# Performance work log

Hardware: AMD Instinct MI355X
Metric: run time of the kernel (lower is better)

The kernel has to match this reference:

```python
import jax, jax.numpy as jnp
import numpy as np
from jax import lax

NUM_STATES = 1024
NUM_OBS = 512
BATCH = 64
SEQ = 128


def setup_inputs() -> dict:
    key = jax.random.key(0)
    k1, k2, k3, k4 = jax.random.split(key, 4)
    value = jax.random.randint(k1, (BATCH, SEQ), 0, NUM_OBS)  # int observation ids
    prior_logits = jax.random.normal(k2, (NUM_STATES,), dtype=jnp.float32)
    trans_logits = jax.random.normal(k3, (NUM_STATES, NUM_STATES), dtype=jnp.float32)
    emission_logits = jax.random.normal(k4, (NUM_STATES, NUM_OBS), dtype=jnp.float32)
    return {"value": value, "prior_logits": prior_logits,
            "trans_logits": trans_logits, "emission_logits": emission_logits}


def reference(value, prior_logits, trans_logits, emission_logits):
    # Categorical(...).logits in torch is log-normalized: logits - logsumexp(logits)
    prior_ln = jax.nn.log_softmax(prior_logits)                 # [S]
    trans_ln = jax.nn.log_softmax(trans_logits, axis=-1)        # [S_from, S_to], row-normalized
    emis_ln = jax.nn.log_softmax(emission_logits, axis=-1)      # [S, V]
    transT = trans_ln.T                                         # [S_to, S_from]

    # Per-timestep emission log-likelihoods: emis_ln[:, value] -> [S, B, T] -> [T, B, S]
    e = jnp.transpose(emis_ln[:, value], (2, 1, 0))

    alpha0 = e[0] + prior_ln                                    # [B, S]

    def step(alpha, e_t):
        # alpha_new[b, j] = e_t[b, j] + logsumexp_i(transT[j, i] + alpha[b, i])
        a = e_t + jax.nn.logsumexp(transT[None, :, :] + alpha[:, None, :], axis=2)
        return a, None

    alpha_final, _ = lax.scan(step, alpha0, e[1:])
    return jax.nn.logsumexp(alpha_final, axis=1)                # [B]
```

## Files before the change

### kernel.cpp

```cpp
#include <hip/hip_runtime.h>
#include <hip/hip_bf16.h>


typedef __attribute__((ext_vector_type(8))) short short8;
typedef __attribute__((ext_vector_type(4))) float f32x4;

__device__ __forceinline__ float bf2f(short x) {
  unsigned u = ((unsigned)(unsigned short)x) << 16;
  return __builtin_bit_cast(float, u);
}
__device__ __forceinline__ short f2bf(float f) {
  unsigned u = __builtin_bit_cast(unsigned, f);
  u += 0x7fffu + ((u >> 16) & 1u);
  return (short)(u >> 16);
}
__device__ __forceinline__ float waveReduceMax(float v) {
  #pragma unroll
  for (int d = 1; d < 64; d <<= 1) v = fmaxf(v, __shfl_xor(v, d, 64));
  return v;
}
__device__ __forceinline__ float waveReduceSum(float v) {
  #pragma unroll
  for (int d = 1; d < 64; d <<= 1) v += __shfl_xor(v, d, 64);
  return v;
}

__device__ __forceinline__ void store_bf16_coh(short* p, short v) {
  asm volatile("global_store_short %0, %1, off sc0 sc1" :: "v"(p), "v"(v) : "memory");
}
__device__ __forceinline__ void store_u32_coh(unsigned* p, unsigned v) {
  asm volatile("global_store_dword %0, %1, off sc0 sc1" :: "v"(p), "v"(v) : "memory");
}
__device__ __forceinline__ unsigned load_u32_coh(const unsigned* p) {
  unsigned r;
  asm volatile("global_load_dword %0, %1, off sc0 sc1\n\ts_waitcnt vmcnt(0)"
               : "=v"(r) : "v"(p) : "memory");
  return r;
}
__device__ __forceinline__ short8 load_short8_coh(const short* p) {
  short8 r;
  asm volatile("global_load_dwordx4 %0, %1, off sc0 sc1\n\ts_waitcnt vmcnt(0)"
               : "=v"(r) : "v"(p) : "memory");
  return r;
}


__global__ __launch_bounds__(256) void k_rowstat(const float* __restrict__ x,
                                                 float* __restrict__ rstat) {
  __shared__ float sm[8];
  const int row = blockIdx.x;
  const float* p = x + row * 1024;
  const int tid = threadIdx.x;
  float m = -1e30f;
  for (int i = tid; i < 1024; i += 256) m = fmaxf(m, p[i]);
  m = waveReduceMax(m);
  if ((tid & 63) == 0) sm[tid >> 6] = m;
  __syncthreads();
  m = fmaxf(fmaxf(sm[0], sm[1]), fmaxf(sm[2], sm[3]));
  float s = 0.f;
  for (int i = tid; i < 1024; i += 256) s += __expf(p[i] - m);
  s = waveReduceSum(s);
  if ((tid & 63) == 0) sm[4 + (tid >> 6)] = s;
  __syncthreads();
  if (tid == 0) {
    float tot = sm[4] + sm[5] + sm[6] + sm[7];
    rstat[row * 2] = m;
    rstat[row * 2 + 1] = 1.0f / tot;
  }
}

__global__ __launch_bounds__(256) void k_fillP(const float* __restrict__ trans,
                                               const float* __restrict__ rstat,
                                               short* __restrict__ P_frag) {
  __shared__ float st[512];
  const int w = blockIdx.x, tid = threadIdx.x;
  for (int kk = 0; kk < 32; ++kk) {
    for (int idx = tid; idx < 512; idx += 256) {
      int il = idx >> 4, jl = idx & 15;
      int i = kk * 32 + il, j = w * 16 + jl;
      float m = rstat[i * 2], invs = rstat[i * 2 + 1];
      st[idx] = __expf(trans[i * 1024 + j] - m) * invs;
    }
    __syncthreads();
    for (int idx = tid; idx < 512; idx += 256) {
      int lane = idx >> 3, e = idx & 7;
      int il = ((lane >> 4) & 3) * 8 + e, jl = lane & 15;
      P_frag[w * 16384 + kk * 512 + idx] = f2bf(st[il * 16 + jl]);
    }
    __syncthreads();
  }
}

__global__ __launch_bounds__(256) void k_emis(const float* __restrict__ x,
                                              short* __restrict__ o) {
  __shared__ float sm[8];
  const int row = blockIdx.x;
  const float* p = x + row * 512;
  const int tid = threadIdx.x;
  float m = -1e30f;
  for (int i = tid; i < 512; i += 256) m = fmaxf(m, p[i]);
  m = waveReduceMax(m);
  if ((tid & 63) == 0) sm[tid >> 6] = m;
  __syncthreads();
  m = fmaxf(fmaxf(sm[0], sm[1]), fmaxf(sm[2], sm[3]));
  float s = 0.f;
  for (int i = tid; i < 512; i += 256) s += __expf(p[i] - m);
  s = waveReduceSum(s);
  if ((tid & 63) == 0) sm[4 + (tid >> 6)] = s;
  __syncthreads();
  float invs = 512.0f / (sm[4] + sm[5] + sm[6] + sm[7]);
  for (int i = tid; i < 512; i += 256)
    o[i * 1024 + row] = f2bf(__expf(p[i] - m) * invs);
}

__global__ __launch_bounds__(256) void k_prior(const float* __restrict__ x,
                                               float* __restrict__ o) {
  __shared__ float sm[8];
  const int tid = threadIdx.x;
  float m = -1e30f;
  for (int i = tid; i < 1024; i += 256) m = fmaxf(m, x[i]);
  m = waveReduceMax(m);
  if ((tid & 63) == 0) sm[tid >> 6] = m;
  __syncthreads();
  m = fmaxf(fmaxf(sm[0], sm[1]), fmaxf(sm[2], sm[3]));
  float s = 0.f;
  for (int i = tid; i < 1024; i += 256) s += __expf(x[i] - m);
  s = waveReduceSum(s);
  if ((tid & 63) == 0) sm[4 + (tid >> 6)] = s;
  __syncthreads();
  float invs = 1.0f / (sm[4] + sm[5] + sm[6] + sm[7]);
  for (int i = tid; i < 1024; i += 256) o[i] = __expf(x[i] - m) * invs;
}


#define LA(OFF) asm volatile("global_load_dwordx4 %0, %1, off offset:" #OFF " sc0 sc1" \
                             : "=v"(a[OFF / 64]) : "v"(ab) : "memory")

__global__ __launch_bounds__(256, 1) void hmm_main(
    const int* __restrict__ value, const float* __restrict__ prior_p,
    const short* __restrict__ P_frag, const short* __restrict__ emisT,
    short* __restrict__ albuf, unsigned int* __restrict__ flg,
    float* __restrict__ out) {
  __shared__ __align__(16) short p_lds[65536];
  __shared__ int v_lds[128 * 16];

  const int bx = blockIdx.x;
  const int d = bx & 3;
  const int m = bx >> 2;
  const int tid = threadIdx.x;
  const int lane = tid & 63;
  const int wid = tid >> 6;
  const int jl = lane & 15;
  const int kg = lane >> 4;
  const int jcol = (m * 4 + wid) * 16 + jl;
  const int bloc0 = kg * 4;

  {
    const short8* src = (const short8*)P_frag + m * 8192;
    short8* dst = (short8*)p_lds;
    #pragma unroll
    for (int i = 0; i < 32; ++i) dst[tid + i * 256] = src[tid + i * 256];
  }
  for (int i = tid; i < 2048; i += 256) {
    int bl = i >> 7, tt = i & 127;
    v_lds[tt * 16 + bl] = value[(d * 16 + bl) * 128 + tt];
  }
  __syncthreads();

  {
    float pj = prior_p[jcol];
    #pragma unroll
    for (int r = 0; r < 4; ++r) {
      int obs = v_lds[bloc0 + r];
      float E = bf2f(emisT[obs * 1024 + jcol]);
      store_bf16_coh(albuf + (d * 16 + bloc0 + r) * 1024 + jcol, f2bf(pj * E));
    }
    asm volatile("s_waitcnt vmcnt(0)" ::: "memory");
    __syncthreads();
    if (tid == 0) store_u32_coh(&flg[d * 2048 + 0 * 16 + m], 1u);
  }

  const short* abase0 = albuf + (d * 16 + jl) * 1024 + kg * 8;
  const short8* bb = (const short8*)p_lds + wid * 2048 + lane;

  for (int t = 1; t < 128; ++t) {
    float Ev[4];
    #pragma unroll
    for (int r = 0; r < 4; ++r) {
      int obs = v_lds[t * 16 + bloc0 + r];
      Ev[r] = bf2f(emisT[obs * 1024 + jcol]);
    }

    if (wid == 0) {
      const unsigned* fp = flg + d * 2048 + (t - 1) * 16 + (lane & 15);
      int tries = 0;
      while (true) {
        unsigned f = load_u32_coh(fp);
        if (__all((int)(f == (unsigned)t))) break;
        if (++tries > (1 << 17)) break;
      }
    }
    __syncthreads();

    const void* ab = (const void*)(abase0 + ((t - 1) & 1) * 65536);
    short8 a[32];
    LA(0);    LA(64);   LA(128);  LA(192);  LA(256);  LA(320);  LA(384);  LA(448);
    LA(512);  LA(576);  LA(640);  LA(704);  LA(768);  LA(832);  LA(896);  LA(960);
    LA(1024); LA(1088); LA(1152); LA(1216); LA(1280); LA(1344); LA(1408); LA(1472);
    LA(1536); LA(1600); LA(1664); LA(1728); LA(1792); LA(1856); LA(1920); LA(1984);
    asm volatile("s_waitcnt vmcnt(0)" ::: "memory");
    __builtin_amdgcn_sched_barrier(0);

    f32x4 acc0 = {0.f, 0.f, 0.f, 0.f}, acc1 = {0.f, 0.f, 0.f, 0.f};
    #pragma unroll
    for (int kk = 0; kk < 32; kk += 2) {
      acc0 = __builtin_amdgcn_mfma_f32_16x16x32_bf16(a[kk], bb[kk * 64], acc0, 0, 0, 0);
      acc1 = __builtin_amdgcn_mfma_f32_16x16x32_bf16(a[kk + 1], bb[(kk + 1) * 64], acc1, 0, 0, 0);
    }

    short* acur = albuf + (t & 1) * 65536;
    #pragma unroll
    for (int r = 0; r < 4; ++r) {
      float sv = (acc0[r] + acc1[r]) * Ev[r];
      store_bf16_coh(acur + (d * 16 + bloc0 + r) * 1024 + jcol, f2bf(sv));
    }
    asm volatile("s_waitcnt vmcnt(0)" ::: "memory");
    __syncthreads();
    if (tid == 0) store_u32_coh(&flg[d * 2048 + t * 16 + m], (unsigned)(t + 1));
  }

  if (m != 0) return;
  if (wid == 0) {
    const unsigned* fp = flg + d * 2048 + 127 * 16 + (lane & 15);
    int tries = 0;
    while (true) {
      unsigned f = load_u32_coh(fp);
      if (__all((int)(f == 128u))) break;
      if (++tries > (1 << 17)) break;
    }
  }
  __syncthreads();
  {
    int row = tid >> 4, chunk = tid & 15;
    const short* base = albuf + 65536 + (d * 16 + row) * 1024 + chunk * 64;
    float s = 0.f;
    #pragma unroll
    for (int q = 0; q < 8; ++q) {
      short8 v = load_short8_coh(base + q * 8);
      #pragma unroll
      for (int e = 0; e < 8; ++e) s += bf2f(v[e]);
    }
    #pragma unroll
    for (int msk = 1; msk < 16; msk <<= 1) s += __shfl_xor(s, msk, 64);
    if (chunk == 0) out[d * 16 + row] = logf(s) - 798.5055520050569f;
  }
}

extern "C" void kernel_launch(void* const* d_in, const int* in_sizes, int n_in,
                              void* d_out, int out_size, void* d_ws, size_t ws_size,
                              hipStream_t stream) {
  const int* value = (const int*)d_in[0];
  const float* prior = (const float*)d_in[1];
  const float* trans = (const float*)d_in[2];
  const float* emis = (const float*)d_in[3];
  char* ws = (char*)d_ws;
  short* P_frag = (short*)(ws + 0x000000);
  short* emisT = (short*)(ws + 0x200000);
  float* prior_p = (float*)(ws + 0x300000);
  float* rstat = (float*)(ws + 0x301000);
  short* albuf = (short*)(ws + 0x310000);
  unsigned* flg = (unsigned*)(ws + 0x350000);
  float* out = (float*)d_out;

  k_rowstat<<<1024, 256, 0, stream>>>(trans, rstat);
  k_fillP<<<64, 256, 0, stream>>>(trans, rstat, P_frag);
  k_emis<<<1024, 256, 0, stream>>>(emis, emisT);
  k_prior<<<1, 256, 0, stream>>>(prior, prior_p);
  hmm_main<<<64, 256, 0, stream>>>(value, prior_p, P_frag, emisT, albuf, flg, out);
}
```

Measured before the change: 828.7 us.

## Coalesce alpha stores via LDS, add per-timestep alpha buffers, prefetch emissions

Each block now stages its 16x64 bf16 alpha tile in LDS and writes it out as 16-byte coherent stores from 128 threads, replacing scattered 2-byte stores. When the workspace is large enough, a templated DEEP path gives every timestep its own alpha buffer and reads it with ordinary cached loads instead of sc0/sc1 coherent loads, so each buffer is written once and never reused. Emission values for the next step are fetched after the flag store, moving that latency off the critical path. The risks are stale cached reads if address uniqueness does not guarantee freshness, an extra __syncthreads per step, and a workspace of about 16 MB.

```diff
diff --git a/kernel.cpp b/kernel.cpp
--- a/kernel.cpp
+++ b/kernel.cpp
@@ -4,6 +4,9 @@
 
 typedef __attribute__((ext_vector_type(8))) short short8;
 typedef __attribute__((ext_vector_type(4))) float f32x4;
+
+#define ALBUF_OFF 0x310000
+#define DEEP_WS_NEED (ALBUF_OFF + 128 * 131072)
 
 __device__ __forceinline__ float bf2f(short x) {
   unsigned u = ((unsigned)(unsigned short)x) << 16;
@@ -25,9 +28,6 @@
   return v;
 }
 
-__device__ __forceinline__ void store_bf16_coh(short* p, short v) {
-  asm volatile("global_store_short %0, %1, off sc0 sc1" :: "v"(p), "v"(v) : "memory");
-}
 __device__ __forceinline__ void store_u32_coh(unsigned* p, unsigned v) {
   asm volatile("global_store_dword %0, %1, off sc0 sc1" :: "v"(p), "v"(v) : "memory");
 }
@@ -37,11 +37,8 @@
                : "=v"(r) : "v"(p) : "memory");
   return r;
 }
-__device__ __forceinline__ short8 load_short8_coh(const short* p) {
-  short8 r;
-  asm volatile("global_load_dwordx4 %0, %1, off sc0 sc1\n\ts_waitcnt vmcnt(0)"
-               : "=v"(r) : "v"(p) : "memory");
-  return r;
+__device__ __forceinline__ void store_short8_coh(short* p, short8 v) {
+  asm volatile("global_store_dwordx4 %0, %1, off sc0 sc1" :: "v"(p), "v"(v) : "memory");
 }
 
 
@@ -133,9 +130,10 @@
 }
 
 
-#define LA(OFF) asm volatile("global_load_dwordx4 %0, %1, off offset:" #OFF " sc0 sc1" \
-                             : "=v"(a[OFF / 64]) : "v"(ab) : "memory")
-
+#define LAU(OFF) asm volatile("global_load_dwordx4 %0, %1, off offset:" #OFF " sc0 sc1" \
+                              : "=v"(a[OFF / 64]) : "v"(ab) : "memory")
+
+template <bool DEEP>
 __global__ __launch_bounds__(256, 1) void hmm_main(
     const int* __restrict__ value, const float* __restrict__ prior_p,
     const short* __restrict__ P_frag, const short* __restrict__ emisT,
@@ -143,6 +141,7 @@
     float* __restrict__ out) {
   __shared__ __align__(16) short p_lds[65536];
   __shared__ int v_lds[128 * 16];
+  __shared__ __align__(16) short o_lds[16 * 80];
 
   const int bx = blockIdx.x;
   const int d = bx & 3;
@@ -152,7 +151,7 @@
   const int wid = tid >> 6;
   const int jl = lane & 15;
   const int kg = lane >> 4;
-  const int jcol = (m * 4 + wid) * 16 + jl;
+  const int jcol = m * 64 + wid * 16 + jl;
   const int bloc0 = kg * 4;
 
   {
@@ -172,25 +171,28 @@
     #pragma unroll
     for (int r = 0; r < 4; ++r) {
       int obs = v_lds[bloc0 + r];
-      float E = bf2f(emisT[obs * 1024 + jcol]);
-      store_bf16_coh(albuf + (d * 16 + bloc0 + r) * 1024 + jcol, f2bf(pj * E));
+      float sv = pj * bf2f(emisT[obs * 1024 + jcol]);
+      o_lds[(bloc0 + r) * 80 + wid * 16 + jl] = f2bf(sv);
+    }
+    __syncthreads();
+    if (tid < 128) {
+      int row = tid >> 3, chunk = tid & 7;
+      short8 v = *(const short8*)(o_lds + row * 80 + chunk * 8);
+      store_short8_coh(albuf + (size_t)(d * 16 + row) * 1024 + m * 64 + chunk * 8, v);
     }
     asm volatile("s_waitcnt vmcnt(0)" ::: "memory");
     __syncthreads();
     if (tid == 0) store_u32_coh(&flg[d * 2048 + 0 * 16 + m], 1u);
   }
 
-  const short* abase0 = albuf + (d * 16 + jl) * 1024 + kg * 8;
   const short8* bb = (const short8*)p_lds + wid * 2048 + lane;
 
+  float Ev[4];
+  #pragma unroll
+  for (int r = 0; r < 4; ++r)
+    Ev[r] = bf2f(emisT[v_lds[1 * 16 + bloc0 + r] * 1024 + jcol]);
+
   for (int t = 1; t < 128; ++t) {
-    float Ev[4];
-    #pragma unroll
-    for (int r = 0; r < 4; ++r) {
-      int obs = v_lds[t * 16 + bloc0 + r];
-      Ev[r] = bf2f(emisT[obs * 1024 + jcol]);
-    }
-
     if (wid == 0) {
       const unsigned* fp = flg + d * 2048 + (t - 1) * 16 + (lane & 15);
       int tries = 0;
@@ -202,31 +204,54 @@
     }
     __syncthreads();
 
-    const void* ab = (const void*)(abase0 + ((t - 1) & 1) * 65536);
     short8 a[32];
-    LA(0);    LA(64);   LA(128);  LA(192);  LA(256);  LA(320);  LA(384);  LA(448);
-    LA(512);  LA(576);  LA(640);  LA(704);  LA(768);  LA(832);  LA(896);  LA(960);
-    LA(1024); LA(1088); LA(1152); LA(1216); LA(1280); LA(1344); LA(1408); LA(1472);
-    LA(1536); LA(1600); LA(1664); LA(1728); LA(1792); LA(1856); LA(1920); LA(1984);
-    asm volatile("s_waitcnt vmcnt(0)" ::: "memory");
-    __builtin_amdgcn_sched_barrier(0);
-
     f32x4 acc0 = {0.f, 0.f, 0.f, 0.f}, acc1 = {0.f, 0.f, 0.f, 0.f};
+    if (DEEP) {
+      const short8* ab8 = (const short8*)(albuf + (size_t)(t - 1) * 65536 +
+                                          (d * 16 + jl) * 1024 + kg * 8);
+      #pragma unroll
+      for (int kk = 0; kk < 32; ++kk) a[kk] = ab8[kk * 4];
+    } else {
+      const void* ab = (const void*)(albuf + (size_t)((t - 1) & 1) * 65536 +
+                                     (d * 16 + jl) * 1024 + kg * 8);
+      LAU(0);    LAU(64);   LAU(128);  LAU(192);  LAU(256);  LAU(320);  LAU(384);  LAU(448);
+      LAU(512);  LAU(576);  LAU(640);  LAU(704);  LAU(768);  LAU(832);  LAU(896);  LAU(960);
+      LAU(1024); LAU(1088); LAU(1152); LAU(1216); LAU(1280); LAU(1344); LAU(1408); LAU(1472);
+      LAU(1536); LAU(1600); LAU(1664); LAU(1728); LAU(1792); LAU(1856); LAU(1920); LAU(1984);
+      asm volatile("s_waitcnt vmcnt(0)" ::: "memory");
+      __builtin_amdgcn_sched_barrier(0);
+    }
+
     #pragma unroll
     for (int kk = 0; kk < 32; kk += 2) {
       acc0 = __builtin_amdgcn_mfma_f32_16x16x32_bf16(a[kk], bb[kk * 64], acc0, 0, 0, 0);
       acc1 = __builtin_amdgcn_mfma_f32_16x16x32_bf16(a[kk + 1], bb[(kk + 1) * 64], acc1, 0, 0, 0);
     }
 
-    short* acur = albuf + (t & 1) * 65536;
     #pragma unroll
     for (int r = 0; r < 4; ++r) {
       float sv = (acc0[r] + acc1[r]) * Ev[r];
-      store_bf16_coh(acur + (d * 16 + bloc0 + r) * 1024 + jcol, f2bf(sv));
-    }
-    asm volatile("s_waitcnt vmcnt(0)" ::: "memory");
+      o_lds[(bloc0 + r) * 80 + wid * 16 + jl] = f2bf(sv);
+    }
+    __syncthreads();
+    {
+      size_t slot = DEEP ? (size_t)t : (size_t)(t & 1);
+      if (tid < 128) {
+        int row = tid >> 3, chunk = tid & 7;
+        short8 v = *(const short8*)(o_lds + row * 80 + chunk * 8);
+        store_short8_coh(albuf + slot * 65536 + (size_t)(d * 16 + row) * 1024 +
+                         m * 64 + chunk * 8, v);
+      }
+      asm volatile("s_waitcnt vmcnt(0)" ::: "memory");
+    }
     __syncthreads();
     if (tid == 0) store_u32_coh(&flg[d * 2048 + t * 16 + m], (unsigned)(t + 1));
+
+    if (t < 127) {
+      #pragma unroll
+      for (int r = 0; r < 4; ++r)
+        Ev[r] = bf2f(emisT[v_lds[(t + 1) * 16 + bloc0 + r] * 1024 + jcol]);
+    }
   }
 
   if (m != 0) return;
@@ -241,18 +266,20 @@
   }
   __syncthreads();
   {
-    int row = tid >> 4, chunk = tid & 15;
-    const short* base = albuf + 65536 + (d * 16 + row) * 1024 + chunk * 64;
+    size_t slot = DEEP ? (size_t)127 : (size_t)1;
+    int row = tid >> 4, seg = tid & 15;
+    const short8* base = (const short8*)(albuf + slot * 65536 +
+                                         (size_t)(d * 16 + row) * 1024 + seg * 64);
     float s = 0.f;
     #pragma unroll
     for (int q = 0; q < 8; ++q) {
-      short8 v = load_short8_coh(base + q * 8);
+      short8 v = base[q];
       #pragma unroll
       for (int e = 0; e < 8; ++e) s += bf2f(v[e]);
     }
     #pragma unroll
     for (int msk = 1; msk < 16; msk <<= 1) s += __shfl_xor(s, msk, 64);
-    if (chunk == 0) out[d * 16 + row] = logf(s) - 798.5055520050569f;
+    if ((lane & 15) == 0) out[d * 16 + row] = logf(s) - 798.5055520050569f;
   }
 }
 
@@ -268,13 +295,17 @@
   short* emisT = (short*)(ws + 0x200000);
   float* prior_p = (float*)(ws + 0x300000);
   float* rstat = (float*)(ws + 0x301000);
-  short* albuf = (short*)(ws + 0x310000);
-  unsigned* flg = (unsigned*)(ws + 0x350000);
+  unsigned* flg = (unsigned*)(ws + 0x303000);
+  short* albuf = (short*)(ws + ALBUF_OFF);
   float* out = (float*)d_out;
 
   k_rowstat<<<1024, 256, 0, stream>>>(trans, rstat);
   k_fillP<<<64, 256, 0, stream>>>(trans, rstat, P_frag);
   k_emis<<<1024, 256, 0, stream>>>(emis, emisT);
   k_prior<<<1, 256, 0, stream>>>(prior, prior_p);
-  hmm_main<<<64, 256, 0, stream>>>(value, prior_p, P_frag, emisT, albuf, flg, out);
-}
+  if (ws_size >= (size_t)DEEP_WS_NEED) {
+    hmm_main<true><<<64, 256, 0, stream>>>(value, prior_p, P_frag, emisT, albuf, flg, out);
+  } else {
+    hmm_main<false><<<64, 256, 0, stream>>>(value, prior_p, P_frag, emisT, albuf, flg, out);
+  }
+}
```

Result: faster. 747.1 us (-9.8%).
